# Optimization experiments

Measured on AMD Instinct MI355X. Metric: run time of the kernel, lower is better.

The kernel has to match this reference:

```python
import jax, jax.numpy as jnp
import numpy as np

DIM = 1024
NUM_HEADS = 16
HEAD_DIM = 64
EPS = 1e-6

def setup_inputs() -> dict:
    key = jax.random.key(0)
    ks = jax.random.split(key, 6)
    x = jax.random.normal(ks[0], (4, 2048, DIM), dtype=jnp.float32)
    # Linear weights stored as (in, out); torch nn.Linear computes x @ W.T with W (out,in),
    # equivalent math with our (in,out) layout.
    Wq = jax.random.normal(ks[1], (DIM, NUM_HEADS * HEAD_DIM), dtype=jnp.float32) / np.sqrt(DIM)
    Wk = jax.random.normal(ks[2], (DIM, NUM_HEADS * HEAD_DIM), dtype=jnp.float32) / np.sqrt(DIM)
    Wv = jax.random.normal(ks[3], (DIM, NUM_HEADS * HEAD_DIM), dtype=jnp.float32) / np.sqrt(DIM)
    Wo = jax.random.normal(ks[4], (NUM_HEADS * HEAD_DIM, DIM), dtype=jnp.float32) / np.sqrt(NUM_HEADS * HEAD_DIM)
    # FeatureMap buffer: randn(head_dim, head_dim)/sqrt(head_dim)
    proj = jax.random.normal(ks[5], (HEAD_DIM, HEAD_DIM), dtype=jnp.float32) / np.sqrt(HEAD_DIM)
    return {"x": x, "Wq": Wq, "Wk": Wk, "Wv": Wv, "Wo": Wo, "proj": proj}

def _feature_map(x, proj):
    # phi(x) = elu(x @ proj) + 1  (positive features)
    return jax.nn.elu(x @ proj) + 1.0

def reference(x, Wq, Wk, Wv, Wo, proj):
    B, S, _ = x.shape
    H, D = NUM_HEADS, HEAD_DIM
    q = (x @ Wq).reshape(B, S, H, D)
    k = (x @ Wk).reshape(B, S, H, D)
    v = (x @ Wv).reshape(B, S, H, D)
    q = _feature_map(q, proj)
    k = _feature_map(k, proj)
    # scan over time: carry kv_state (B,H,D,D) and k_state (B,H,D)
    q_t = jnp.moveaxis(q, 1, 0)  # (S,B,H,D)
    k_t = jnp.moveaxis(k, 1, 0)
    v_t = jnp.moveaxis(v, 1, 0)

    def step(carry, qkv):
        kv, ksum = carry
        qt, kt, vt = qkv  # each (B,H,D)
        kv = kv + kt[..., :, None] * vt[..., None, :]  # outer product k v^T
        ksum = ksum + kt
        num = jnp.einsum('bhd,bhde->bhe', qt, kv)
        den = jnp.einsum('bhd,bhd->bh', qt, ksum) + EPS
        return (kv, ksum), num / den[..., None]

    kv0 = jnp.zeros((B, H, D, D), dtype=x.dtype)
    ks0 = jnp.zeros((B, H, D), dtype=x.dtype)
    _, out = jax.lax.scan(step, (kv0, ks0), (q_t, k_t, v_t))
    out = jnp.moveaxis(out, 0, 1).reshape(B, S, H * D)  # (B,S,H*D)
    return out @ Wo
```

## Files before the change

kernel.cpp:

```cpp
#include <hip/hip_runtime.h>

typedef unsigned short u16;
typedef unsigned int   u32;
typedef short bfrag8 __attribute__((ext_vector_type(8)));
typedef float facc4  __attribute__((ext_vector_type(4)));

#define DIM    1024
#define NH     16
#define HD     64
#define BSZ    4
#define SEQ    2048
#define MROWS  (BSZ*SEQ)
#define CHUNK  64
#define NCHUNK (SEQ/CHUNK)
#define BH     (BSZ*NH)
#define TS     72
#define NT     16

#define BARRIER() asm volatile("s_barrier" ::: "memory")

__device__ __forceinline__ u16 f2bf(float f) {
  u32 u = __builtin_bit_cast(u32, f);
  u32 r = u + 0x7fffu + ((u >> 16) & 1u);
  return (u16)(r >> 16);
}
__device__ __forceinline__ float bf2f(u16 b) {
  return __builtin_bit_cast(float, (u32)b << 16);
}

__device__ __forceinline__ void gload_lds16(const void* g, void* l) {
  __builtin_amdgcn_global_load_lds((const __attribute__((address_space(1))) u32*)g,
                                   (__attribute__((address_space(3))) u32*)l, 16, 0, 0);
}


__global__ __launch_bounds__(256) void conv_f32_bf16(const float* __restrict__ in, u16* __restrict__ out) {
  const int i = (blockIdx.x * 256 + threadIdx.x) * 4;
  const float4 v = *(const float4*)(in + i);
  ushort4 o;
  o.x = f2bf(v.x); o.y = f2bf(v.y); o.z = f2bf(v.z); o.w = f2bf(v.w);
  *(ushort4*)(out + i) = o;
}

__global__ __launch_bounds__(256) void fold_qk(const float* __restrict__ Wq, const float* __restrict__ Wk,
                                               const float* __restrict__ proj, u16* __restrict__ wt) {
  const int i0 = blockIdx.x * 32;
  const int h  = blockIdx.y;
  const int sel = blockIdx.z;
  const float* W = sel ? Wk : Wq;
  u16* out = wt + (size_t)sel * (DIM*DIM);
  __shared__ float sp[64*64];
  __shared__ float sw[32*64];
  const int tid = threadIdx.x;
  for (int idx = tid; idx < 4096; idx += 256) sp[idx] = proj[idx];
  for (int idx = tid; idx < 2048; idx += 256) {
    int r = idx >> 6, c = idx & 63;
    sw[idx] = W[(size_t)(i0 + r)*DIM + h*64 + c];
  }
  __syncthreads();
  const int i  = tid >> 3;
  const int e0 = (tid & 7) * 8;
  #pragma unroll
  for (int ee = 0; ee < 8; ++ee) {
    const int e = e0 + ee;
    float acc = 0.f;
    for (int d = 0; d < 64; ++d) acc += sw[i*64 + d] * sp[d*64 + e];
    out[(size_t)(h*64 + e)*DIM + i0 + i] = f2bf(acc);
  }
}

__global__ __launch_bounds__(256) void trans_conv(const float* __restrict__ Wv, const float* __restrict__ Wo,
                                                  u16* __restrict__ wt) {
  const int sel = blockIdx.z;
  const float* in = sel ? Wo : Wv;
  u16* out = wt + (size_t)(2 + sel) * (DIM*DIM);
  const int n0 = blockIdx.x * 32, k0 = blockIdx.y * 32;
  __shared__ float tile[32][33];
  const int tid = threadIdx.x;
  for (int idx = tid; idx < 1024; idx += 256) {
    int r = idx >> 5, c = idx & 31;
    tile[r][c] = in[(size_t)(k0 + r)*DIM + n0 + c];
  }
  __syncthreads();
  for (int idx = tid; idx < 1024; idx += 256) {
    int r = idx >> 5, c = idx & 31;
    out[(size_t)(n0 + r)*DIM + k0 + c] = f2bf(tile[c][r]);
  }
}

#define OPENB()  { BARRIER(); asm volatile("s_waitcnt lgkmcnt(0)" ::: "memory"); __builtin_amdgcn_sched_barrier(0); }
#define CLOSEB() { __builtin_amdgcn_sched_barrier(0); BARRIER(); }

#define RD_X(MH) { _Pragma("unroll") for (int mf = 0; mf < 4; ++mf) { \
    _Pragma("unroll") for (int kh = 0; kh < 2; ++kh) { \
      const int row = (MH)*128 + wm*64 + mf*16 + lr; \
      xf[mf*2+kh] = *(const bfrag8*)&lX[row*64 + (((kh*4+g) ^ (row & 7)) << 3)]; } } }

#define RD_W(NHH) { _Pragma("unroll") for (int nf = 0; nf < 2; ++nf) { \
    _Pragma("unroll") for (int kh = 0; kh < 2; ++kh) { \
      const int row = (NHH)*128 + wn*32 + nf*16 + lr; \
      wf[(NHH)*4 + nf*2+kh] = *(const bfrag8*)&lW[row*64 + (((kh*4+g) ^ (row & 7)) << 3)]; } } }

#define MM(MH, NHH) { __builtin_amdgcn_s_setprio(1); \
    _Pragma("unroll") for (int nf = 0; nf < 2; ++nf) { \
    _Pragma("unroll") for (int mf = 0; mf < 4; ++mf) { \
    _Pragma("unroll") for (int kh = 0; kh < 2; ++kh) { \
      acc[(NHH)*2+nf][(MH)*4+mf] = __builtin_amdgcn_mfma_f32_16x16x32_bf16( \
          wf[(NHH)*4+nf*2+kh], xf[mf*2+kh], acc[(NHH)*2+nf][(MH)*4+mf], 0, 0, 0); } } } \
    __builtin_amdgcn_s_setprio(0); }

template<int MODE>
__global__ __launch_bounds__(512, 1)
void gemm8p(const u16* __restrict__ A, const u16* __restrict__ W,
            u16* __restrict__ outb, float* __restrict__ outf) {
  __shared__ u16 lds[2][32768];
  const int tid  = threadIdx.x;
  const int wave = tid >> 6, lane = tid & 63;
  const int wm = wave >> 2, wn = wave & 3;
  const int lr = lane & 15, g = lane >> 4;

  const int NYv = (MODE == 0) ? 12 : 4;
  const int q   = gridDim.x >> 3;
  const int nf_ = ((int)blockIdx.x & 7) * q + ((int)blockIdx.x >> 3);
  const int m0  = (nf_ / NYv) * 256;
  const int ngl = (nf_ % NYv) * 256;

  auto stage = [&](const u16* mat, int rowbase, int kt, int isW, int h) {
    #pragma unroll
    for (int o = 0; o < 2; ++o) {
      const int s = o*512 + tid;
      const int rih = s >> 3, sl = s & 7;
      gload_lds16(mat + (size_t)(rowbase + h*128 + rih)*DIM + kt*64 + ((sl ^ (rih & 7)) << 3),
                  &lds[kt & 1][isW*16384 + h*8192 + (o*512 + wave*64)*8]);
    }
  };

  stage(A, m0, 0, 0, 0);
  stage(W, ngl, 0, 1, 0);
  stage(A, m0, 0, 0, 1);
  stage(W, ngl, 0, 1, 1);
  stage(A, m0, 1, 0, 0);
  stage(W, ngl, 1, 1, 1);
  asm volatile("s_waitcnt vmcnt(4)" ::: "memory");
  BARRIER();

  facc4 acc[4][8] = {};

  for (int t = 0; t < NT; ++t) {
    const u16* lX = &lds[t & 1][0];
    const u16* lW = &lds[t & 1][16384];
    bfrag8 xf[8], wf[8];
    RD_X(0); RD_W(0);
    if (t + 1 < NT) stage(A, m0, t+1, 0, 1);
    OPENB(); MM(0,0); CLOSEB();
    RD_W(1);
    if (t + 1 < NT) stage(W, ngl, t+1, 1, 0);
    OPENB(); MM(0,1); CLOSEB();
    RD_X(1);
    if (t + 2 < NT) stage(A, m0, t+2, 0, 0);
    OPENB(); MM(1,1); CLOSEB();
    if (t + 2 < NT) stage(W, ngl, t+2, 1, 1);
    OPENB(); MM(1,0);
    __builtin_amdgcn_sched_barrier(0);
    if (t + 2 < NT)      asm volatile("s_waitcnt vmcnt(4)" ::: "memory");
    else if (t + 1 < NT) asm volatile("s_waitcnt vmcnt(0)" ::: "memory");
    if (t + 1 < NT) BARRIER();
  }

  const int sel = (MODE == 0) ? (ngl >> 10) : 0;
  const bool doElu = (MODE == 0) && (sel < 2);
  const int coly = (MODE == 0) ? (ngl & 1023) : ngl;
  #pragma unroll
  for (int nh = 0; nh < 2; ++nh) {
    #pragma unroll
    for (int nf = 0; nf < 2; ++nf) {
      #pragma unroll
      for (int mh = 0; mh < 2; ++mh) {
        #pragma unroll
        for (int mf = 0; mf < 4; ++mf) {
          const facc4 a = acc[nh*2+nf][mh*4+mf];
          const int m = m0 + mh*128 + wm*64 + mf*16 + lr;
          const int col0 = coly + nh*128 + wn*32 + nf*16 + g*4;
          float v0 = a[0], v1 = a[1], v2 = a[2], v3 = a[3];
          if (MODE == 0) {
            if (doElu) {
              v0 = (v0 > 0.f) ? (v0 + 1.f) : __expf(v0);
              v1 = (v1 > 0.f) ? (v1 + 1.f) : __expf(v1);
              v2 = (v2 > 0.f) ? (v2 + 1.f) : __expf(v2);
              v3 = (v3 > 0.f) ? (v3 + 1.f) : __expf(v3);
            }
            uint2 pk;
            pk.x = (u32)f2bf(v0) | ((u32)f2bf(v1) << 16);
            pk.y = (u32)f2bf(v2) | ((u32)f2bf(v3) << 16);
            *(uint2*)&outb[(size_t)sel*((size_t)MROWS*DIM) + (size_t)m*DIM + col0] = pk;
          } else {
            float4 pk; pk.x = v0; pk.y = v1; pk.z = v2; pk.w = v3;
            *(float4*)&outf[(size_t)m*DIM + col0] = pk;
          }
        }
      }
    }
  }
}


__global__ __launch_bounds__(256) void phaseA(const u16* __restrict__ Kb, const u16* __restrict__ Vb,
                                              u16* __restrict__ Ast, float* __restrict__ ksum) {
  const int c = blockIdx.x, bh = blockIdx.y;
  const int b = bh >> 4, h = bh & 15;
  const int tid = threadIdx.x;
  const int wave = tid >> 6, lane = tid & 63, lr = lane & 15, g = lane >> 4;
  __shared__ u16 lKt[64*TS];
  __shared__ u16 lVt[64*TS];
  const size_t mbase = (size_t)b*SEQ + (size_t)c*CHUNK;

  for (int s = tid; s < 512; s += 256) {
    const int t = s >> 3, dg = (s & 7) * 8;
    const bfrag8 kk = *(const bfrag8*)&Kb[(mbase + t)*DIM + h*64 + dg];
    const bfrag8 vv = *(const bfrag8*)&Vb[(mbase + t)*DIM + h*64 + dg];
    #pragma unroll
    for (int j = 0; j < 8; ++j) {
      lKt[(dg + j)*TS + t] = (u16)kk[j];
      lVt[(dg + j)*TS + t] = (u16)vv[j];
    }
  }
  __syncthreads();

  facc4 acc[4] = {};
  #pragma unroll
  for (int kt = 0; kt < 2; ++kt) {
    const bfrag8 af = *(const bfrag8*)&lVt[(wave*16 + lr)*TS + kt*32 + g*8];
    #pragma unroll
    for (int j = 0; j < 4; ++j) {
      const bfrag8 bk = *(const bfrag8*)&lKt[(j*16 + lr)*TS + kt*32 + g*8];
      acc[j] = __builtin_amdgcn_mfma_f32_16x16x32_bf16(af, bk, acc[j], 0, 0, 0);
    }
  }
  u16* dst = Ast + (((size_t)bh*NCHUNK + c) << 12);
  #pragma unroll
  for (int j = 0; j < 4; ++j)
    #pragma unroll
    for (int r = 0; r < 4; ++r)
      dst[(wave*16 + g*4 + r)*64 + j*16 + lr] = f2bf(acc[j][r]);

  const int d = tid >> 2, seg = tid & 3;
  const bfrag8 k0 = *(const bfrag8*)&lKt[d*TS + seg*16];
  const bfrag8 k1 = *(const bfrag8*)&lKt[d*TS + seg*16 + 8];
  float s = 0.f;
  #pragma unroll
  for (int j = 0; j < 8; ++j) s += bf2f((u16)k0[j]) + bf2f((u16)k1[j]);
  s += __shfl_xor(s, 1, 64);
  s += __shfl_xor(s, 2, 64);
  if (seg == 0) ksum[((size_t)bh*NCHUNK + c)*64 + d] = s;
}

__global__ __launch_bounds__(256) void phaseB(u16* __restrict__ Ast, float* __restrict__ ksum) {
  const int bh = blockIdx.x, slice = blockIdx.y;
  const int tid = threadIdx.x;
  u16* base = Ast + (size_t)bh*NCHUNK*4096 + slice*256 + tid;
  float v[NCHUNK];
  #pragma unroll
  for (int c = 0; c < NCHUNK; ++c) v[c] = bf2f(base[(size_t)c*4096]);
  float run = 0.f;
  #pragma unroll
  for (int c = 0; c < NCHUNK; ++c) { base[(size_t)c*4096] = f2bf(run); run += v[c]; }
  if (slice == 0 && tid < 64) {
    float rs = 0.f;
    float* kp = ksum + (size_t)bh*NCHUNK*64 + tid;
    for (int c = 0; c < NCHUNK; ++c) { const float t = kp[c*64]; kp[c*64] = rs; rs += t; }
  }
}

__global__ __launch_bounds__(256) void phaseC(const u16* __restrict__ Qb, const u16* __restrict__ Kb,
                                              const u16* __restrict__ Vb, const u16* __restrict__ Ast,
                                              const float* __restrict__ ksum, u16* __restrict__ Ob) {
  const int c = blockIdx.x, bh = blockIdx.y;
  const int b = bh >> 4, h = bh & 15;
  const int tid = threadIdx.x;
  const int wave = tid >> 6, lane = tid & 63, lr = lane & 15, g = lane >> 4;
  __shared__ u16 lS  [64*TS];
  __shared__ u16 lVt [64*TS];
  __shared__ u16 lKVt[64*TS];
  __shared__ float lks[64];
  __shared__ float lrs[64];
  __shared__ float lqk[64];
  const size_t mbase = (size_t)b*SEQ + (size_t)c*CHUNK;

  for (int s = tid; s < 512; s += 256) {
    const int t = s >> 3, dg = (s & 7) * 8;
    const bfrag8 vv = *(const bfrag8*)&Vb[(mbase + t)*DIM + h*64 + dg];
    #pragma unroll
    for (int j = 0; j < 8; ++j) lVt[(dg + j)*TS + t] = (u16)vv[j];
  }
  const u16* kvsrc = Ast + (((size_t)bh*NCHUNK + c) << 12);
  for (int s = tid; s < 512; s += 256) {
    const int e = s >> 3, dg = (s & 7) * 8;
    *(bfrag8*)&lKVt[e*TS + dg] = *(const bfrag8*)&kvsrc[e*64 + dg];
  }
  if (tid < 64) lks[tid] = ksum[((size_t)bh*NCHUNK + c)*64 + tid];

  bfrag8 qf[2], kf[4][2];
  {
    const u16* qrow = Qb + (mbase + wave*16 + lr)*DIM + h*64;
    qf[0] = *(const bfrag8*)&qrow[g*8];
    qf[1] = *(const bfrag8*)&qrow[32 + g*8];
  }
  #pragma unroll
  for (int j = 0; j < 4; ++j) {
    const u16* krow = Kb + (mbase + j*16 + lr)*DIM + h*64;
    kf[j][0] = *(const bfrag8*)&krow[g*8];
    kf[j][1] = *(const bfrag8*)&krow[32 + g*8];
  }

  facc4 accs[4] = {};
  #pragma unroll
  for (int kt = 0; kt < 2; ++kt)
    #pragma unroll
    for (int j = 0; j < 4; ++j)
      accs[j] = __builtin_amdgcn_mfma_f32_16x16x32_bf16(qf[kt], kf[j][kt], accs[j], 0, 0, 0);

  float rs[4] = {0.f, 0.f, 0.f, 0.f};
  #pragma unroll
  for (int j = 0; j < 4; ++j) {
    const int cc = j*16 + lr;
    #pragma unroll
    for (int r = 0; r < 4; ++r) {
      const int rr = wave*16 + g*4 + r;
      const float vS = (cc <= rr) ? accs[j][r] : 0.f;
      rs[r] += vS;
      lS[rr*TS + cc] = f2bf(vS);
    }
  }
  #pragma unroll
  for (int r = 0; r < 4; ++r) {
    float t = rs[r];
    t += __shfl_xor(t, 1, 64); t += __shfl_xor(t, 2, 64);
    t += __shfl_xor(t, 4, 64); t += __shfl_xor(t, 8, 64);
    if (lr == 0) lrs[wave*16 + g*4 + r] = t;
  }
  __syncthreads();

  {
    const u16* qr2 = Qb + (mbase + wave*16 + lr)*DIM + h*64 + g*16;
    const bfrag8 a0 = *(const bfrag8*)&qr2[0];
    const bfrag8 a1 = *(const bfrag8*)&qr2[8];
    float t = 0.f;
    #pragma unroll
    for (int j = 0; j < 8; ++j)
      t += bf2f((u16)a0[j]) * lks[g*16 + j] + bf2f((u16)a1[j]) * lks[g*16 + 8 + j];
    t += __shfl_xor(t, 16, 64);
    t += __shfl_xor(t, 32, 64);
    if (g == 0) lqk[wave*16 + lr] = t;
  }

  facc4 acco[4] = {};
  #pragma unroll
  for (int kt = 0; kt < 2; ++kt) {
    const bfrag8 sf = *(const bfrag8*)&lS[(wave*16 + lr)*TS + kt*32 + g*8];
    #pragma unroll
    for (int j = 0; j < 4; ++j) {
      const bfrag8 vf = *(const bfrag8*)&lVt[(j*16 + lr)*TS + kt*32 + g*8];
      acco[j] = __builtin_amdgcn_mfma_f32_16x16x32_bf16(sf, vf, acco[j], 0, 0, 0);
    }
  }
  #pragma unroll
  for (int kt = 0; kt < 2; ++kt)
    #pragma unroll
    for (int j = 0; j < 4; ++j) {
      const bfrag8 kvf = *(const bfrag8*)&lKVt[(j*16 + lr)*TS + kt*32 + g*8];
      acco[j] = __builtin_amdgcn_mfma_f32_16x16x32_bf16(qf[kt], kvf, acco[j], 0, 0, 0);
    }

  #pragma unroll
  for (int r = 0; r < 4; ++r) {
    const int rr = wave*16 + g*4 + r;
    const float rden = 1.0f / (lrs[rr] + lqk[rr] + 1e-6f);
    #pragma unroll
    for (int j = 0; j < 4; ++j)
      Ob[(mbase + rr)*DIM + h*64 + j*16 + lr] = f2bf(acco[j][r] * rden);
  }
}

extern "C" void kernel_launch(void* const* d_in, const int* in_sizes, int n_in,
                              void* d_out, int out_size, void* d_ws, size_t ws_size,
                              hipStream_t stream) {
  const float* x    = (const float*)d_in[0];
  const float* Wq   = (const float*)d_in[1];
  const float* Wk   = (const float*)d_in[2];
  const float* Wv   = (const float*)d_in[3];
  const float* Wo   = (const float*)d_in[4];
  const float* proj = (const float*)d_in[5];
  float* out = (float*)d_out;

  char* ws = (char*)d_ws;
  u16*   xb   = (u16*)  (ws);
  u16*   wt   = (u16*)  (ws + 16777216);
  u16*   qkv  = (u16*)  (ws + 25165824);
  u16*   Ob   = (u16*)  (ws + 75497472);
  u16*   Ast  = (u16*)  (ws + 92274688);
  float* ksum = (float*)(ws + 109051904);
  (void)ws_size; (void)in_sizes; (void)n_in; (void)out_size;

  conv_f32_bf16<<<dim3((MROWS*DIM)/1024), 256, 0, stream>>>(x, xb);
  fold_qk      <<<dim3(DIM/32, NH, 2), 256, 0, stream>>>(Wq, Wk, proj, wt);
  trans_conv   <<<dim3(DIM/32, DIM/32, 2), 256, 0, stream>>>(Wv, Wo, wt);

  gemm8p<0><<<dim3(32*12), 512, 0, stream>>>(xb, wt, qkv, nullptr);

  const u16* Qb = qkv;
  const u16* Kb = qkv + (size_t)MROWS*DIM;
  const u16* Vb = qkv + 2*(size_t)MROWS*DIM;

  phaseA<<<dim3(NCHUNK, BH), 256, 0, stream>>>(Kb, Vb, Ast, ksum);
  phaseB<<<dim3(BH, 16), 256, 0, stream>>>(Ast, ksum);
  phaseC<<<dim3(NCHUNK, BH), 256, 0, stream>>>(Qb, Kb, Vb, Ast, ksum, Ob);

  gemm8p<1><<<dim3(32*4), 512, 0, stream>>>(Ob, wt + 3*(size_t)DIM*DIM, nullptr, out);
}
```

Before: 195.3 us.

## Shrink GEMM tile to 128x256 and restructure LDS double-buffer pipeline

Both GEMMs switch from a 256x256 block tile to a 128x256 tile, which doubles the grid size (768 and 256 blocks) and cuts LDS use and accumulator registers in half. The K-loop is rebuilt as a two-phase double buffer in which the whole next k-tile is prefetched during the current one, replacing the earlier four-step schedule that staged data two tiles ahead. The aim is better CU occupancy and load balance, since the output GEMM previously launched only 128 blocks on a 256-CU part. In exchange, operand reuse per block drops and more global/L2 traffic is spent on reloading W tiles.

Result: faster. 186.9 us (-4.3%).

```diff
diff --git a/kernel.cpp b/kernel.cpp
--- a/kernel.cpp
+++ b/kernel.cpp
@@ -18,6 +18,7 @@
 #define NT     16
 
 #define BARRIER() asm volatile("s_barrier" ::: "memory")
+#define OPENB()  { BARRIER(); asm volatile("s_waitcnt lgkmcnt(0)" ::: "memory"); __builtin_amdgcn_sched_barrier(0); }
 
 __device__ __forceinline__ u16 f2bf(float f) {
   u32 u = __builtin_bit_cast(u32, f);
@@ -88,83 +89,89 @@
   }
 }
 
-#define OPENB()  { BARRIER(); asm volatile("s_waitcnt lgkmcnt(0)" ::: "memory"); __builtin_amdgcn_sched_barrier(0); }
-#define CLOSEB() { __builtin_amdgcn_sched_barrier(0); BARRIER(); }
-
-#define RD_X(MH) { _Pragma("unroll") for (int mf = 0; mf < 4; ++mf) { \
-    _Pragma("unroll") for (int kh = 0; kh < 2; ++kh) { \
-      const int row = (MH)*128 + wm*64 + mf*16 + lr; \
-      xf[mf*2+kh] = *(const bfrag8*)&lX[row*64 + (((kh*4+g) ^ (row & 7)) << 3)]; } } }
-
-#define RD_W(NHH) { _Pragma("unroll") for (int nf = 0; nf < 2; ++nf) { \
-    _Pragma("unroll") for (int kh = 0; kh < 2; ++kh) { \
-      const int row = (NHH)*128 + wn*32 + nf*16 + lr; \
-      wf[(NHH)*4 + nf*2+kh] = *(const bfrag8*)&lW[row*64 + (((kh*4+g) ^ (row & 7)) << 3)]; } } }
-
-#define MM(MH, NHH) { __builtin_amdgcn_s_setprio(1); \
-    _Pragma("unroll") for (int nf = 0; nf < 2; ++nf) { \
-    _Pragma("unroll") for (int mf = 0; mf < 4; ++mf) { \
-    _Pragma("unroll") for (int kh = 0; kh < 2; ++kh) { \
-      acc[(NHH)*2+nf][(MH)*4+mf] = __builtin_amdgcn_mfma_f32_16x16x32_bf16( \
-          wf[(NHH)*4+nf*2+kh], xf[mf*2+kh], acc[(NHH)*2+nf][(MH)*4+mf], 0, 0, 0); } } } \
-    __builtin_amdgcn_s_setprio(0); }
-
 template<int MODE>
 __global__ __launch_bounds__(512, 1)
-void gemm8p(const u16* __restrict__ A, const u16* __restrict__ W,
-            u16* __restrict__ outb, float* __restrict__ outf) {
-  __shared__ u16 lds[2][32768];
+void gemmA(const u16* __restrict__ A, const u16* __restrict__ W,
+           u16* __restrict__ outb, float* __restrict__ outf) {
+  __shared__ u16 lds[2][24576];
   const int tid  = threadIdx.x;
   const int wave = tid >> 6, lane = tid & 63;
   const int wm = wave >> 2, wn = wave & 3;
   const int lr = lane & 15, g = lane >> 4;
 
-  const int NYv = (MODE == 0) ? 12 : 4;
-  const int q   = gridDim.x >> 3;
-  const int nf_ = ((int)blockIdx.x & 7) * q + ((int)blockIdx.x >> 3);
-  const int m0  = (nf_ / NYv) * 256;
-  const int ngl = (nf_ % NYv) * 256;
-
-  auto stage = [&](const u16* mat, int rowbase, int kt, int isW, int h) {
-    #pragma unroll
-    for (int o = 0; o < 2; ++o) {
-      const int s = o*512 + tid;
-      const int rih = s >> 3, sl = s & 7;
-      gload_lds16(mat + (size_t)(rowbase + h*128 + rih)*DIM + kt*64 + ((sl ^ (rih & 7)) << 3),
-                  &lds[kt & 1][isW*16384 + h*8192 + (o*512 + wave*64)*8]);
-    }
+  const int NY  = (MODE == 0) ? 12 : 4;
+  const int q   = (int)gridDim.x >> 3;
+  const int bid = (int)blockIdx.x;
+  const int nf_ = (bid & 7) * q + (bid >> 3);
+  const int m0  = (nf_ / NY) * 128;
+  const int ngl = (nf_ % NY) * 256;
+
+  auto stage = [&](const u16* mat, int rowbase, int kt, int isW, int seg) {
+    const int rih = tid >> 3, sl = tid & 7;
+    gload_lds16(mat + (size_t)(rowbase + seg*64 + rih)*DIM + kt*64 + ((sl ^ (rih & 7)) << 3),
+                &lds[kt & 1][isW*8192 + seg*4096 + tid*8]);
   };
 
-  stage(A, m0, 0, 0, 0);
-  stage(W, ngl, 0, 1, 0);
-  stage(A, m0, 0, 0, 1);
-  stage(W, ngl, 0, 1, 1);
-  stage(A, m0, 1, 0, 0);
-  stage(W, ngl, 1, 1, 1);
-  asm volatile("s_waitcnt vmcnt(4)" ::: "memory");
+  stage(A, m0, 0, 0, 0); stage(A, m0, 0, 0, 1);
+  stage(W, ngl, 0, 1, 0); stage(W, ngl, 0, 1, 1); stage(W, ngl, 0, 1, 2); stage(W, ngl, 0, 1, 3);
+  asm volatile("s_waitcnt vmcnt(0)" ::: "memory");
   BARRIER();
 
-  facc4 acc[4][8] = {};
+  facc4 acc[4][4] = {};
+  bfrag8 xf[8], wf[4];
 
   for (int t = 0; t < NT; ++t) {
     const u16* lX = &lds[t & 1][0];
-    const u16* lW = &lds[t & 1][16384];
-    bfrag8 xf[8], wf[8];
-    RD_X(0); RD_W(0);
-    if (t + 1 < NT) stage(A, m0, t+1, 0, 1);
-    OPENB(); MM(0,0); CLOSEB();
-    RD_W(1);
-    if (t + 1 < NT) stage(W, ngl, t+1, 1, 0);
-    OPENB(); MM(0,1); CLOSEB();
-    RD_X(1);
-    if (t + 2 < NT) stage(A, m0, t+2, 0, 0);
-    OPENB(); MM(1,1); CLOSEB();
-    if (t + 2 < NT) stage(W, ngl, t+2, 1, 1);
-    OPENB(); MM(1,0);
+    const u16* lW = &lds[t & 1][8192];
+    #pragma unroll
+    for (int mf = 0; mf < 4; ++mf)
+      #pragma unroll
+      for (int kh = 0; kh < 2; ++kh) {
+        const int row = wm*64 + mf*16 + lr;
+        xf[mf*2+kh] = *(const bfrag8*)&lX[row*64 + (((kh*4+g) ^ (row & 7)) << 3)];
+      }
+    #pragma unroll
+    for (int nf = 0; nf < 2; ++nf)
+      #pragma unroll
+      for (int kh = 0; kh < 2; ++kh) {
+        const int row = wn*32 + nf*16 + lr;
+        wf[nf*2+kh] = *(const bfrag8*)&lW[row*64 + (((kh*4+g) ^ (row & 7)) << 3)];
+      }
+    if (t + 1 < NT) { stage(A, m0, t+1, 0, 0); stage(A, m0, t+1, 0, 1); stage(W, ngl, t+1, 1, 0); }
+    OPENB();
+    __builtin_amdgcn_s_setprio(1);
+    #pragma unroll
+    for (int nf = 0; nf < 2; ++nf)
+      #pragma unroll
+      for (int mf = 0; mf < 4; ++mf)
+        #pragma unroll
+        for (int kh = 0; kh < 2; ++kh)
+          acc[nf][mf] = __builtin_amdgcn_mfma_f32_16x16x32_bf16(wf[nf*2+kh], xf[mf*2+kh], acc[nf][mf], 0, 0, 0);
+    __builtin_amdgcn_s_setprio(0);
     __builtin_amdgcn_sched_barrier(0);
-    if (t + 2 < NT)      asm volatile("s_waitcnt vmcnt(4)" ::: "memory");
-    else if (t + 1 < NT) asm volatile("s_waitcnt vmcnt(0)" ::: "memory");
-    if (t + 1 < NT) BARRIER();
+    if (t + 1 < NT) asm volatile("s_waitcnt vmcnt(3)" ::: "memory");
+    else            asm volatile("s_waitcnt vmcnt(0)" ::: "memory");
+    BARRIER();
+    #pragma unroll
+    for (int nf = 0; nf < 2; ++nf)
+      #pragma unroll
+      for (int kh = 0; kh < 2; ++kh) {
+        const int row = 128 + wn*32 + nf*16 + lr;
+        wf[nf*2+kh] = *(const bfrag8*)&lW[row*64 + (((kh*4+g) ^ (row & 7)) << 3)];
+      }
+    if (t + 1 < NT) { stage(W, ngl, t+1, 1, 1); stage(W, ngl, t+1, 1, 2); stage(W, ngl, t+1, 1, 3); }
+    OPENB();
+    __builtin_amdgcn_s_setprio(1);
+    #pragma unroll
+    for (int nf = 0; nf < 2; ++nf)
+      #pragma unroll
+      for (int mf = 0; mf < 4; ++mf)
+        #pragma unroll
+        for (int kh = 0; kh < 2; ++kh)
+          acc[2+nf][mf] = __builtin_amdgcn_mfma_f32_16x16x32_bf16(wf[nf*2+kh], xf[mf*2+kh], acc[2+nf][mf], 0, 0, 0);
+    __builtin_amdgcn_s_setprio(0);
+    __builtin_amdgcn_sched_barrier(0);
+    if (t + 1 < NT) { asm volatile("s_waitcnt vmcnt(2)" ::: "memory"); BARRIER(); }
   }
 
   const int sel = (MODE == 0) ? (ngl >> 10) : 0;
@@ -175,28 +182,25 @@
     #pragma unroll
     for (int nf = 0; nf < 2; ++nf) {
       #pragma unroll
-      for (int mh = 0; mh < 2; ++mh) {
-        #pragma unroll
-        for (int mf = 0; mf < 4; ++mf) {
-          const facc4 a = acc[nh*2+nf][mh*4+mf];
-          const int m = m0 + mh*128 + wm*64 + mf*16 + lr;
-          const int col0 = coly + nh*128 + wn*32 + nf*16 + g*4;
-          float v0 = a[0], v1 = a[1], v2 = a[2], v3 = a[3];
-          if (MODE == 0) {
-            if (doElu) {
-              v0 = (v0 > 0.f) ? (v0 + 1.f) : __expf(v0);
-              v1 = (v1 > 0.f) ? (v1 + 1.f) : __expf(v1);
-              v2 = (v2 > 0.f) ? (v2 + 1.f) : __expf(v2);
-              v3 = (v3 > 0.f) ? (v3 + 1.f) : __expf(v3);
-            }
-            uint2 pk;
-            pk.x = (u32)f2bf(v0) | ((u32)f2bf(v1) << 16);
-            pk.y = (u32)f2bf(v2) | ((u32)f2bf(v3) << 16);
-            *(uint2*)&outb[(size_t)sel*((size_t)MROWS*DIM) + (size_t)m*DIM + col0] = pk;
-          } else {
-            float4 pk; pk.x = v0; pk.y = v1; pk.z = v2; pk.w = v3;
-            *(float4*)&outf[(size_t)m*DIM + col0] = pk;
+      for (int mf = 0; mf < 4; ++mf) {
+        const facc4 a = acc[nh*2+nf][mf];
+        const int m = m0 + wm*64 + mf*16 + lr;
+        const int col0 = coly + nh*128 + wn*32 + nf*16 + g*4;
+        float v0 = a[0], v1 = a[1], v2 = a[2], v3 = a[3];
+        if (MODE == 0) {
+          if (doElu) {
+            v0 = (v0 > 0.f) ? (v0 + 1.f) : __expf(v0);
+            v1 = (v1 > 0.f) ? (v1 + 1.f) : __expf(v1);
+            v2 = (v2 > 0.f) ? (v2 + 1.f) : __expf(v2);
+            v3 = (v3 > 0.f) ? (v3 + 1.f) : __expf(v3);
           }
+          uint2 pk;
+          pk.x = (u32)f2bf(v0) | ((u32)f2bf(v1) << 16);
+          pk.y = (u32)f2bf(v2) | ((u32)f2bf(v3) << 16);
+          *(uint2*)&outb[(size_t)sel*((size_t)MROWS*DIM) + (size_t)m*DIM + col0] = pk;
+        } else {
+          float4 pk; pk.x = v0; pk.y = v1; pk.z = v2; pk.w = v3;
+          *(float4*)&outf[(size_t)m*DIM + col0] = pk;
         }
       }
     }
@@ -405,7 +409,7 @@
   fold_qk      <<<dim3(DIM/32, NH, 2), 256, 0, stream>>>(Wq, Wk, proj, wt);
   trans_conv   <<<dim3(DIM/32, DIM/32, 2), 256, 0, stream>>>(Wv, Wo, wt);
 
-  gemm8p<0><<<dim3(32*12), 512, 0, stream>>>(xb, wt, qkv, nullptr);
+  gemmA<0><<<dim3(64*12), 512, 0, stream>>>(xb, wt, qkv, nullptr);
 
   const u16* Qb = qkv;
   const u16* Kb = qkv + (size_t)MROWS*DIM;
@@ -415,5 +419,5 @@
   phaseB<<<dim3(BH, 16), 256, 0, stream>>>(Ast, ksum);
   phaseC<<<dim3(NCHUNK, BH), 256, 0, stream>>>(Qb, Kb, Vb, Ast, ksum, Ob);
 
-  gemm8p<1><<<dim3(32*4), 512, 0, stream>>>(Ob, wt + 3*(size_t)DIM*DIM, nullptr, out);
-}
+  gemmA<1><<<dim3(64*4), 512, 0, stream>>>(Ob, wt + 3*(size_t)DIM*DIM, nullptr, out);
+}
```
